# Optimization experiments

Hardware: AMD Instinct MI355X
Metric: run time of the kernel (lower is better)

Reference implementation:

```python
import jax, jax.numpy as jnp
import numpy as np

# Model dims (mamba_ssm defaults: expand=2, d_state=16, d_conv=4, dt_rank=ceil(d_model/16))
V, D_MODEL, N_LAYERS = 32000, 768, 2
D_INNER, D_STATE, D_CONV, DT_RANK = 1536, 16, 4, 48
BATCH, SEQ = 2, 2048


def setup_inputs() -> dict:
    key = jax.random.key(0)
    ks = jax.random.split(key, 10)

    def nrm(k, shape, s=0.02):
        return (jax.random.normal(k, shape) * s).astype(jnp.float32)

    x = jax.random.randint(ks[0], (BATCH, SEQ), 0, V)
    emb = nrm(ks[1], (V, D_MODEL))
    # per-layer Mamba params, stacked on leading layer axis
    W_in = nrm(ks[2], (N_LAYERS, 2 * D_INNER, D_MODEL))          # in_proj (no bias)
    conv_w = nrm(ks[3], (N_LAYERS, D_INNER, 1, D_CONV), 0.1)      # depthwise causal conv
    conv_b = jnp.zeros((N_LAYERS, D_INNER), jnp.float32)
    W_x = nrm(ks[4], (N_LAYERS, DT_RANK + 2 * D_STATE, D_INNER))  # x_proj (no bias)
    W_dt = nrm(ks[5], (N_LAYERS, D_INNER, DT_RANK), 0.05)         # dt_proj
    b_dt = jnp.full((N_LAYERS, D_INNER), -4.0, jnp.float32)       # softplus(-4) ~ small dt
    # A initialized as -exp(A_log) with A_log = log(1..d_state), per mamba_ssm
    A_log = jnp.log(jnp.broadcast_to(
        jnp.arange(1, D_STATE + 1, dtype=jnp.float32), (N_LAYERS, D_INNER, D_STATE)))
    D_skip = jnp.ones((N_LAYERS, D_INNER), jnp.float32)
    W_out = nrm(ks[6], (N_LAYERS, D_MODEL, D_INNER))              # out_proj (no bias)
    ln_g = jnp.ones((D_MODEL,), jnp.float32)
    ln_b = jnp.zeros((D_MODEL,), jnp.float32)
    head_w = nrm(ks[7], (V, D_MODEL))
    head_b = jnp.zeros((V,), jnp.float32)
    return dict(x=x, emb=emb, W_in=W_in, conv_w=conv_w, conv_b=conv_b, W_x=W_x,
                W_dt=W_dt, b_dt=b_dt, A_log=A_log, D_skip=D_skip, W_out=W_out,
                ln_g=ln_g, ln_b=ln_b, head_w=head_w, head_b=head_b)


def mamba_block(h, W_in, conv_w, conv_b, W_x, W_dt, b_dt, A_log, D_skip, W_out):
    # h: (B, L, D_MODEL)
    xz = jnp.einsum('bld,ed->ble', h, W_in)              # (B, L, 2*d_inner)
    u, z = jnp.split(xz, 2, axis=-1)
    # causal depthwise conv over time
    uc = jnp.transpose(u, (0, 2, 1))                     # (B, d_inner, L)
    uc = jax.lax.conv_general_dilated(
        uc, conv_w, window_strides=(1,), padding=[(D_CONV - 1, 0)],
        feature_group_count=D_INNER, dimension_numbers=('NCH', 'OIH', 'NCH'))
    u = jax.nn.silu(jnp.transpose(uc, (0, 2, 1)) + conv_b)
    # input-dependent dt, B, C
    x_dbl = jnp.einsum('bld,ed->ble', u, W_x)            # (B, L, dt_rank+2*d_state)
    dtl, Bm, Cm = jnp.split(x_dbl, [DT_RANK, DT_RANK + D_STATE], axis=-1)
    dt = jax.nn.softplus(jnp.einsum('blr,dr->bld', dtl, W_dt) + b_dt)  # (B, L, d_inner)
    A = -jnp.exp(A_log)                                  # (d_inner, d_state)

    def step(hst, inp):
        dt_t, u_t, B_t, C_t = inp                        # (B,d_inner),(B,d_inner),(B,d_state),(B,d_state)
        hst = jnp.exp(dt_t[..., None] * A) * hst + (dt_t * u_t)[..., None] * B_t[:, None, :]
        y_t = jnp.einsum('bds,bs->bd', hst, C_t)
        return hst, y_t

    h0 = jnp.zeros((u.shape[0], D_INNER, D_STATE), u.dtype)
    xs = (dt.transpose(1, 0, 2), u.transpose(1, 0, 2),
          Bm.transpose(1, 0, 2), Cm.transpose(1, 0, 2))
    _, ys = jax.lax.scan(step, h0, xs)                   # (L, B, d_inner)
    y = ys.transpose(1, 0, 2) + u * D_skip
    y = y * jax.nn.silu(z)
    return jnp.einsum('bli,oi->blo', y, W_out)           # back to (B, L, D_MODEL)


def reference(x, emb, W_in, conv_w, conv_b, W_x, W_dt, b_dt, A_log, D_skip,
              W_out, ln_g, ln_b, head_w, head_b):
    h = emb[x]                                           # (B, L, D_MODEL)
    for l in range(N_LAYERS):
        h = h + mamba_block(h, W_in[l], conv_w[l], conv_b[l], W_x[l], W_dt[l],
                            b_dt[l], A_log[l], D_skip[l], W_out[l])
    mu = jnp.mean(h, axis=-1, keepdims=True)
    var = jnp.mean((h - mu) ** 2, axis=-1, keepdims=True)
    hn = (h - mu) * jax.lax.rsqrt(var + 1e-5) * ln_g + ln_b
    return jnp.einsum('bld,vd->blv', hn, head_w) + head_b
```

## Files before the change

kernel.cpp:

```cpp
#include <hip/hip_runtime.h>
#include <hip/hip_bf16.h>
#include <stdint.h>

#define BL    4096
#define DM    768
#define DI    1536
#define DS    16
#define DCONV 4
#define DTR   48
#define NL    2
#define SEQL  2048
#define BATCH 2
#define VOC   32000
#define NCH   32
#define CT    64

typedef __bf16 bf16_t;
typedef __bf16 bf16x8 __attribute__((ext_vector_type(8)));
typedef __bf16 bf16x4 __attribute__((ext_vector_type(4)));
typedef float  f32x4  __attribute__((ext_vector_type(4)));

__device__ __forceinline__ float sigmoidf_(float x) { return 1.f / (1.f + __expf(-x)); }
__device__ __forceinline__ float softplus_(float x) {
  return (x > 20.f) ? x : log1pf(__expf(x));
}

__global__ __launch_bounds__(256) void k_embed(const int* __restrict__ x,
                                               const float* __restrict__ emb,
                                               float* __restrict__ h,
                                               bf16_t* __restrict__ hb) {
  int row = blockIdx.x;
  int tok = x[row];
  const float* e = emb + (size_t)tok * DM;
  float* hr = h + (size_t)row * DM;
  bf16_t* hbr = hb + (size_t)row * DM;
  for (int c = threadIdx.x; c < DM; c += 256) {
    float v = e[c];
    hr[c] = v;
    hbr[c] = (bf16_t)v;
  }
}

#define NV0 1179648L
#define NV1 589824L
#define NV2 6144000L
#define NS3 393216L
#define NS4 196608L
#define NVT (NV0 + NV1 + NV2)
#define NTOT (NVT + NS3 + NS4)

__global__ __launch_bounds__(256) void k_cvtw(const float* __restrict__ Win,
                                              const float* __restrict__ Wout,
                                              const float* __restrict__ Whead,
                                              const float* __restrict__ Wx,
                                              const float* __restrict__ Wdt,
                                              bf16_t* __restrict__ bin,
                                              bf16_t* __restrict__ bout,
                                              bf16_t* __restrict__ bhead,
                                              bf16_t* __restrict__ bx,
                                              bf16_t* __restrict__ bdt) {
  long i = (long)blockIdx.x * 256 + threadIdx.x;
  if (i >= NTOT) return;
  if (i < NVT) {
    const float* s; bf16_t* d; long j = i;
    if (i < NV0)            { s = Win;   d = bin; }
    else if (i < NV0 + NV1) { s = Wout;  d = bout;  j = i - NV0; }
    else                    { s = Whead; d = bhead; j = i - NV0 - NV1; }
    float4 v = ((const float4*)s)[j];
    bf16x4 o;
    o[0] = (bf16_t)v.x; o[1] = (bf16_t)v.y; o[2] = (bf16_t)v.z; o[3] = (bf16_t)v.w;
    ((bf16x4*)d)[j] = o;
  } else if (i < NVT + NS3) {
    long j = i - NVT;
    int l = (int)(j / (128 * 1536));
    int rr = (int)((j / 1536) % 128);
    int c = (int)(j % 1536);
    bx[j] = (bf16_t)(rr < 80 ? Wx[((long)l * 80 + rr) * 1536 + c] : 0.f);
  } else {
    long j = i - NVT - NS3;
    int l = (int)(j / (1536 * 64));
    int r = (int)((j / 64) % 1536);
    int c = (int)(j & 63);
    bdt[j] = (bf16_t)(c < DTR ? Wdt[((long)l * 1536 + r) * DTR + c] : 0.f);
  }
}

__global__ __launch_bounds__(256) void k_cvt_pad(const float* __restrict__ src,
                                                 bf16_t* __restrict__ dst,
                                                 int R, int C, int srcLd, int Cpad,
                                                 long total) {
  long i = (long)blockIdx.x * 256 + threadIdx.x;
  if (i >= total) return;
  int r = (int)(i / Cpad), c = (int)(i % Cpad);
  float v = (r < R && c < C) ? src[(size_t)r * srcLd + c] : 0.f;
  dst[i] = (bf16_t)v;
}

__global__ __launch_bounds__(256) void k_zero(float* __restrict__ p, long n4) {
  long i = (long)blockIdx.x * 256 + threadIdx.x;
  if (i < n4) ((float4*)p)[i] = (float4){0.f, 0.f, 0.f, 0.f};
}

__global__ __launch_bounds__(256) void k_conv(const float* __restrict__ xz,
                                              const float* __restrict__ cw,
                                              const float* __restrict__ cb,
                                              bf16_t* __restrict__ ucb, long total) {
  long i = (long)blockIdx.x * 256 + threadIdx.x;
  if (i >= total) return;
  int d = (int)(i % DI);
  long row = i / DI;
  int l = (int)(row % SEQL);
  const float* w = cw + (size_t)d * DCONV;
  float s = cb[d];
#pragma unroll
  for (int j = 0; j < DCONV; j++) {
    int lj = l - (DCONV - 1) + j;
    if (lj >= 0) s += xz[(row - (DCONV - 1) + j) * (2 * DI) + d] * w[j];
  }
  float v = s * sigmoidf_(s);
  ucb[i] = (bf16_t)v;
}

__global__ __launch_bounds__(256) void k_scan1(const float* __restrict__ dt,
                                               const bf16_t* __restrict__ uc,
                                               const float* __restrict__ xdbl,
                                               const float* __restrict__ A_log,
                                               float* __restrict__ cA,
                                               float* __restrict__ cB) {
  int gi = blockIdx.x * 256 + threadIdx.x;
  int s = gi & 15;
  int rest = gi >> 4;
  int d = rest % DI;
  int rest2 = rest / DI;
  int c = rest2 % NCH;
  int b = rest2 / NCH;
  float a = -__expf(A_log[d * DS + s]);
  long l0 = (long)c * CT;
  const float*  dtp = dt + ((long)b * SEQL + l0) * DI + d;
  const bf16_t* ucp = uc + ((long)b * SEQL + l0) * DI + d;
  const float*  Bp  = xdbl + ((long)b * SEQL + l0) * 80 + DTR + s;
  float S = 0.f, hh = 0.f;
#pragma unroll 4
  for (int l = 0; l < CT; l++) {
    float dtv = dtp[(long)l * DI];
    float uv  = (float)ucp[(long)l * DI];
    float Bv  = Bp[(long)l * 80];
    S += dtv;
    hh = __expf(dtv * a) * hh + (dtv * uv) * Bv;
  }
  cA[gi] = __expf(a * S);
  cB[gi] = hh;
}

__global__ __launch_bounds__(256) void k_scan2(const float* __restrict__ cA,
                                               const float* __restrict__ cB,
                                               float* __restrict__ hst) {
  int gj = blockIdx.x * 256 + threadIdx.x;
  int ds_ = gj & (DI * DS - 1);
  int b = gj / (DI * DS);
  float h = 0.f;
#pragma unroll
  for (int c = 0; c < NCH; c++) {
    long idx = ((long)(b * NCH + c) * DI * DS) + ds_;
    hst[idx] = h;
    h = cA[idx] * h + cB[idx];
  }
}

__global__ __launch_bounds__(256) void k_scan3g(const float* __restrict__ dt,
                                                const bf16_t* uc,
                                                const float* __restrict__ xdbl,
                                                const float* __restrict__ A_log,
                                                const float* __restrict__ hst,
                                                const float* __restrict__ xz,
                                                const float* __restrict__ Dsk,
                                                bf16_t* o) {
  int gi = blockIdx.x * 256 + threadIdx.x;
  int s = gi & 15;
  int rest = gi >> 4;
  int d = rest % DI;
  int rest2 = rest / DI;
  int c = rest2 % NCH;
  int b = rest2 / NCH;
  float a = -__expf(A_log[d * DS + s]);
  float dval = Dsk[d];
  long l0 = (long)c * CT;
  const float*  dtp = dt + ((long)b * SEQL + l0) * DI + d;
  const bf16_t* ucp = uc + ((long)b * SEQL + l0) * DI + d;
  const float*  Bp  = xdbl + ((long)b * SEQL + l0) * 80 + DTR + s;
  const float*  Cp  = Bp + DS;
  const float*  zp  = xz + ((long)b * SEQL + l0) * (2 * DI) + DI + d;
  bf16_t* yp = o + ((long)b * SEQL + l0) * DI + d;
  float h = hst[gi];
#pragma unroll 4
  for (int l = 0; l < CT; l++) {
    float dtv = dtp[(long)l * DI];
    float uv  = (float)ucp[(long)l * DI];
    float Bv  = Bp[(long)l * 80];
    float Cv  = Cp[(long)l * 80];
    h = __expf(dtv * a) * h + (dtv * uv) * Bv;
    float y = h * Cv;
    y += __shfl_xor(y, 1);
    y += __shfl_xor(y, 2);
    y += __shfl_xor(y, 4);
    y += __shfl_xor(y, 8);
    if (s == 0) {
      float z = zp[(long)l * 2 * DI];
      float yy = (y + uv * dval) * z * sigmoidf_(z);
      yp[(long)l * DI] = (bf16_t)yy;
    }
  }
}

__global__ __launch_bounds__(256) void k_ln(const float* __restrict__ h,
                                            const float* __restrict__ g,
                                            const float* __restrict__ bta,
                                            bf16_t* __restrict__ o) {
  __shared__ float sm[4];
  int row = blockIdx.x;
  int t = threadIdx.x;
  const float* hr = h + (long)row * DM;
  float v0 = hr[t], v1 = hr[t + 256], v2 = hr[t + 512];
  float s = v0 + v1 + v2;
#pragma unroll
  for (int off = 32; off > 0; off >>= 1) s += __shfl_down(s, off);
  if ((t & 63) == 0) sm[t >> 6] = s;
  __syncthreads();
  float mu = (sm[0] + sm[1] + sm[2] + sm[3]) * (1.f / DM);
  __syncthreads();
  float d0 = v0 - mu, d1 = v1 - mu, d2 = v2 - mu;
  float q = d0 * d0 + d1 * d1 + d2 * d2;
#pragma unroll
  for (int off = 32; off > 0; off >>= 1) q += __shfl_down(q, off);
  if ((t & 63) == 0) sm[t >> 6] = q;
  __syncthreads();
  float var = (sm[0] + sm[1] + sm[2] + sm[3]) * (1.f / DM);
  float rs = rsqrtf(var + 1e-5f);
  bf16_t* orow = o + (long)row * DM;
  orow[t]       = (bf16_t)(d0 * rs * g[t]       + bta[t]);
  orow[t + 256] = (bf16_t)(d1 * rs * g[t + 256] + bta[t + 256]);
  orow[t + 512] = (bf16_t)(d2 * rs * g[t + 512] + bta[t + 512]);
}

__device__ __forceinline__ void stage16(const bf16_t* gp, bf16_t* lp) {
  __builtin_amdgcn_global_load_lds(
      (const __attribute__((address_space(1))) uint32_t*)gp,
      (__attribute__((address_space(3))) uint32_t*)lp, 16, 0, 0);
}

template <int EPI>
__global__ __launch_bounds__(256) void k_gemm(const bf16_t* __restrict__ A,
                                              const bf16_t* __restrict__ W,
                                              float* __restrict__ C,
                                              const float* __restrict__ bias,
                                              bf16_t* __restrict__ side,
                                              int M, int N, int K, int ldc) {
  __shared__ char smem[16384];
  bf16_t* lA = (bf16_t*)smem;
  bf16_t* lB = (bf16_t*)(smem + 8192);
  const int tid = threadIdx.x;
  const int lane = tid & 63;
  const int wv = tid >> 6;
  const int wm = wv >> 1, wn = wv & 1;
  const long m0 = (long)blockIdx.y * 128;
  const long n0 = (long)blockIdx.x * 128;
  const int r0 = tid >> 2;
  const int c8 = (tid & 3) * 8;
  const int fr = lane & 15;
  const int kq = lane >> 4;

  f32x4 acc[4][4];
#pragma unroll
  for (int i = 0; i < 4; i++)
#pragma unroll
    for (int j = 0; j < 4; j++) acc[i][j] = (f32x4){0.f, 0.f, 0.f, 0.f};

  const bf16_t* Ab = A + (m0 + r0) * (long)K + c8;
  const bf16_t* Wb = W + (n0 + r0) * (long)K + c8;
  bf16_t* lAp = lA + r0 * 32 + c8;
  bf16_t* lBp = lB + r0 * 32 + c8;
  const long s64K = 64L * K;

  for (int k0 = 0; k0 < K; k0 += 32) {
    __syncthreads();
    stage16(Ab + k0, lAp);
    stage16(Ab + k0 + s64K, lAp + 64 * 32);
    stage16(Wb + k0, lBp);
    stage16(Wb + k0 + s64K, lBp + 64 * 32);
    __syncthreads();
    bf16x8 af[4], bfv[4];
#pragma unroll
    for (int f = 0; f < 4; f++)
      af[f] = *(const bf16x8*)&lA[(wm * 64 + f * 16 + fr) * 32 + kq * 8];
#pragma unroll
    for (int f = 0; f < 4; f++)
      bfv[f] = *(const bf16x8*)&lB[(wn * 64 + f * 16 + fr) * 32 + kq * 8];
#pragma unroll
    for (int fm = 0; fm < 4; fm++)
#pragma unroll
      for (int fn = 0; fn < 4; fn++)
        acc[fm][fn] = __builtin_amdgcn_mfma_f32_16x16x32_bf16(af[fm], bfv[fn],
                                                              acc[fm][fn], 0, 0, 0);
  }

  {
    float* lf = (float*)smem;
    const int q = lane >> 4;
    const int cc = lane & 15;
    const int colt = (tid & 31) * 4;
    float4 bias4 = {0.f, 0.f, 0.f, 0.f};
    if (EPI == 3) bias4 = *(const float4*)&bias[n0 + colt];
#pragma unroll
    for (int p = 0; p < 4; ++p) {
      __syncthreads();
      if (wm == (p >> 1)) {
#pragma unroll
        for (int fl = 0; fl < 2; ++fl) {
          int fm = (p & 1) * 2 + fl;
#pragma unroll
          for (int fn = 0; fn < 4; ++fn) {
            f32x4 v = acc[fm][fn];
            float* dst = &lf[(fl * 16 + q * 4) * 128 + wn * 64 + fn * 16 + cc];
#pragma unroll
            for (int r = 0; r < 4; ++r) dst[r * 128] = v[r];
          }
        }
      }
      __syncthreads();
      const long rowg0 = m0 + p * 32;
#pragma unroll
      for (int it = 0; it < 4; ++it) {
        int rl = it * 8 + (tid >> 5);
        f32x4 v = *(const f32x4*)&lf[rl * 128 + colt];
        long row = rowg0 + rl;
        long cg = n0 + colt;
        float* gp = &C[row * (long)ldc + cg];
        if (EPI == 3) {
          v[0] = softplus_(v[0] + bias4.x);
          v[1] = softplus_(v[1] + bias4.y);
          v[2] = softplus_(v[2] + bias4.z);
          v[3] = softplus_(v[3] + bias4.w);
          *(f32x4*)gp = v;
        } else {
          f32x4 c0 = *(const f32x4*)gp;
          v[0] += c0[0]; v[1] += c0[1]; v[2] += c0[2]; v[3] += c0[3];
          *(f32x4*)gp = v;
          bf16x4 s4;
          s4[0] = (bf16_t)v[0]; s4[1] = (bf16_t)v[1];
          s4[2] = (bf16_t)v[2]; s4[3] = (bf16_t)v[3];
          *(bf16x4*)&side[row * (long)ldc + cg] = s4;
        }
      }
    }
  }
}

__global__ __launch_bounds__(256) void k_gemm_sk(const bf16_t* __restrict__ A,
                                                 const bf16_t* __restrict__ W,
                                                 float* __restrict__ C,
                                                 int N, int K, int KS, int ldc) {
  __shared__ bf16_t lA[128 * 32];
  __shared__ bf16_t lB[128 * 32];
  const int tid = threadIdx.x;
  const int lane = tid & 63;
  const int wv = tid >> 6;
  const int wm = wv >> 1, wn = wv & 1;
  const long m0 = (long)blockIdx.y * 128;
  const long n0 = (long)blockIdx.x * 128;
  const int kLo = blockIdx.z * KS;
  const int r0 = tid >> 2;
  const int c8 = (tid & 3) * 8;
  const int fr = lane & 15;
  const int kq = lane >> 4;

  f32x4 acc[4][4];
#pragma unroll
  for (int i = 0; i < 4; i++)
#pragma unroll
    for (int j = 0; j < 4; j++) acc[i][j] = (f32x4){0.f, 0.f, 0.f, 0.f};

  const bf16_t* Ab = A + (m0 + r0) * (long)K + c8;
  const bf16_t* Wb = W + (n0 + r0) * (long)K + c8;
  bf16_t* lAp = lA + r0 * 32 + c8;
  bf16_t* lBp = lB + r0 * 32 + c8;
  const long s64K = 64L * K;

  for (int k0 = kLo; k0 < kLo + KS; k0 += 32) {
    __syncthreads();
    stage16(Ab + k0, lAp);
    stage16(Ab + k0 + s64K, lAp + 64 * 32);
    stage16(Wb + k0, lBp);
    stage16(Wb + k0 + s64K, lBp + 64 * 32);
    __syncthreads();
    bf16x8 af[4], bfv[4];
#pragma unroll
    for (int f = 0; f < 4; f++)
      af[f] = *(const bf16x8*)&lA[(wm * 64 + f * 16 + fr) * 32 + kq * 8];
#pragma unroll
    for (int f = 0; f < 4; f++)
      bfv[f] = *(const bf16x8*)&lB[(wn * 64 + f * 16 + fr) * 32 + kq * 8];
#pragma unroll
    for (int fm = 0; fm < 4; fm++)
#pragma unroll
      for (int fn = 0; fn < 4; fn++)
        acc[fm][fn] = __builtin_amdgcn_mfma_f32_16x16x32_bf16(af[fm], bfv[fn],
                                                              acc[fm][fn], 0, 0, 0);
  }

  const int r4 = (lane >> 4) * 4;
  const int cc = lane & 15;
#pragma unroll
  for (int fm = 0; fm < 4; fm++) {
    long rowb = m0 + wm * 64 + fm * 16 + r4;
#pragma unroll
    for (int fn = 0; fn < 4; fn++) {
      long col = n0 + wn * 64 + fn * 16 + cc;
      if (col < N) {
#pragma unroll
        for (int r = 0; r < 4; r++)
          atomicAdd(&C[(rowb + r) * (long)ldc + col], acc[fm][fn][r]);
      }
    }
  }
}


#define GLD256(ab, j, ktt, pp) do {                                             \
    int idx_ = (j) * 512 + tid;                                                 \
    int r_ = idx_ >> 3; int c16_ = idx_ & 7;                                    \
    size_t col_ = (size_t)(ktt) * 64 + (size_t)((c16_ ^ (r_ & 7)) << 3);        \
    const bf16_t* gp_ = (ab) ? (Wp + ((size_t)(n0 + r_)) * K + col_)            \
                             : (Ap + ((size_t)(m0 + r_)) * K + col_);           \
    bf16_t* lp_ = lds + ((((pp) * 2 + (ab)) * 256 + r_) * 64) + c16_ * 8;       \
    __builtin_amdgcn_global_load_lds(                                           \
        (const __attribute__((address_space(1))) uint32_t*)gp_,                 \
        (__attribute__((address_space(3))) uint32_t*)lp_, 16, 0, 0);            \
  } while (0)

#define STAGE_ALL(pp, ktt) do {                                                 \
    GLD256(0, 0, ktt, pp); GLD256(0, 2, ktt, pp);                               \
    GLD256(1, 0, ktt, pp); GLD256(1, 1, ktt, pp);                               \
    GLD256(1, 2, ktt, pp); GLD256(1, 3, ktt, pp);                               \
    GLD256(0, 1, ktt, pp); GLD256(0, 3, ktt, pp);                               \
  } while (0)

#define COMPUTE256(pp, mg, kh) do {                                             \
    const char* lb_ = (const char*)lds;                                         \
    bf16x8 af_[4], bv_[4];                                                      \
    _Pragma("unroll") for (int f = 0; f < 4; ++f) {                             \
      int row_ = wm * 128 + (mg) * 64 + f * 16 + fr;                            \
      int byte_ = (((pp) * 2 + 0) * 256 + row_) * 128 +                         \
                  (((kh) * 64 + kq * 16) ^ ((row_ & 7) << 4));                  \
      af_[f] = *(const bf16x8*)(lb_ + byte_);                                   \
    }                                                                           \
    _Pragma("unroll") for (int f = 0; f < 4; ++f) {                             \
      int row_ = wn * 64 + f * 16 + fr;                                         \
      int byte_ = (((pp) * 2 + 1) * 256 + row_) * 128 +                         \
                  (((kh) * 64 + kq * 16) ^ ((row_ & 7) << 4));                  \
      bv_[f] = *(const bf16x8*)(lb_ + byte_);                                   \
    }                                                                           \
    __builtin_amdgcn_s_setprio(1);                                              \
    _Pragma("unroll") for (int fm = 0; fm < 4; ++fm)                            \
      _Pragma("unroll") for (int fn = 0; fn < 4; ++fn)                          \
        acc[(mg) * 4 + fm][fn] = __builtin_amdgcn_mfma_f32_16x16x32_bf16(       \
            af_[fm], bv_[fn], acc[(mg) * 4 + fm][fn], 0, 0, 0);                 \
    __builtin_amdgcn_s_setprio(0);                                              \
  } while (0)

#define WAITV8()  asm volatile("s_waitcnt vmcnt(8)" ::: "memory")
#define WAITV2()  asm volatile("s_waitcnt vmcnt(2)" ::: "memory")
#define WAITV0()  asm volatile("s_waitcnt vmcnt(0)" ::: "memory")
#define BARRIER() do { __builtin_amdgcn_s_barrier();                            \
                       asm volatile("" ::: "memory"); } while (0)

template <int EPI>
__global__ __launch_bounds__(512, 2) void k_gemm256(const bf16_t* __restrict__ Ap,
                                                    const bf16_t* __restrict__ Wp,
                                                    float* __restrict__ C,
                                                    const float* __restrict__ bias,
                                                    int K, int ldc) {
  __shared__ bf16_t lds[2 * 2 * 256 * 64];
  const int tid = threadIdx.x;
  const int lane = tid & 63;
  const int wid = tid >> 6;
  const int wm = wid >> 2, wn = wid & 3;
  const int fr = lane & 15, kq = lane >> 4;

  const int cpx = gridDim.x >> 3;
  const int wg = ((int)blockIdx.x & 7) * cpx + ((int)blockIdx.x >> 3);
  const long m0 = (long)(wg & 15) * 256;
  const long n0 = (long)(wg >> 4) * 256;

  f32x4 acc[8][4];
#pragma unroll
  for (int i = 0; i < 8; i++)
#pragma unroll
    for (int j = 0; j < 4; j++) acc[i][j] = (f32x4){0.f, 0.f, 0.f, 0.f};

  STAGE_ALL(0, 0);
  WAITV2();
  BARRIER();

  const int NT = K >> 6;
  for (int kt = 0; kt < NT; ++kt) {
    const int p = kt & 1;
    const bool pre = (kt + 1 < NT);
    if (pre) STAGE_ALL(p ^ 1, kt + 1);
    COMPUTE256(p, 0, 0);
    if (pre) WAITV8(); else WAITV0();
    BARRIER();
    COMPUTE256(p, 1, 0);
    COMPUTE256(p, 0, 1);
    COMPUTE256(p, 1, 1);
    if (pre) {
      WAITV2();
      BARRIER();
    }
  }

  {
    float* lf = (float*)(void*)lds;
    const int q = lane >> 4;
    const int cc = lane & 15;
    float4 bias4 = {0.f, 0.f, 0.f, 0.f};
    if (EPI == 1) bias4 = *(const float4*)&bias[n0 + lane * 4];
#pragma unroll
    for (int p = 0; p < 4; ++p) {
      __syncthreads();
      if (wm == (p >> 1)) {
        const int mgb = (p & 1) * 4;
#pragma unroll
        for (int m4 = 0; m4 < 4; ++m4)
#pragma unroll
          for (int n = 0; n < 4; ++n) {
            f32x4 v = acc[mgb + m4][n];
            float* dst = &lf[(m4 * 16 + q * 4) * 260 + wn * 64 + n * 16 + cc];
#pragma unroll
            for (int r = 0; r < 4; ++r) dst[r * 260] = v[r];
          }
      }
      __syncthreads();
      const long rowg0 = m0 + p * 64;
#pragma unroll
      for (int it = 0; it < 8; ++it) {
        int row_loc = wid * 8 + it;
        f32x4 v = *(const f32x4*)&lf[row_loc * 260 + lane * 4];
        float* gp = &C[(rowg0 + row_loc) * (long)ldc + n0 + lane * 4];
        if (EPI == 1) {
          v[0] += bias4.x; v[1] += bias4.y; v[2] += bias4.z; v[3] += bias4.w;
          __builtin_nontemporal_store(v, (f32x4*)gp);
        } else {
          *(f32x4*)gp = v;
        }
      }
    }
  }
}

static inline int cdiv_l(long a, long b) { return (int)((a + b - 1) / b); }

extern "C" void kernel_launch(void* const* d_in, const int* in_sizes, int n_in,
                              void* d_out, int out_size, void* d_ws, size_t ws_size,
                              hipStream_t stream) {
  (void)in_sizes; (void)n_in; (void)out_size; (void)ws_size;
  const int*   x      = (const int*)  d_in[0];
  const float* emb    = (const float*)d_in[1];
  const float* W_in   = (const float*)d_in[2];
  const float* conv_w = (const float*)d_in[3];
  const float* conv_b = (const float*)d_in[4];
  const float* W_x    = (const float*)d_in[5];
  const float* W_dt   = (const float*)d_in[6];
  const float* b_dt   = (const float*)d_in[7];
  const float* A_log  = (const float*)d_in[8];
  const float* D_skip = (const float*)d_in[9];
  const float* W_out  = (const float*)d_in[10];
  const float* ln_g   = (const float*)d_in[11];
  const float* ln_b   = (const float*)d_in[12];
  const float* head_w = (const float*)d_in[13];
  const float* head_b = (const float*)d_in[14];
  float* out = (float*)d_out;

  bf16_t* abuf   = (bf16_t*)d_ws;
  bf16_t* hbf    = abuf   + (size_t)BL * DI;
  bf16_t* dtl    = hbf    + (size_t)BL * DM;
  bf16_t* wb_in  = dtl    + (size_t)BL * 64;
  bf16_t* wb_out = wb_in  + (size_t)2 * 3072 * 768;
  bf16_t* wb_hd  = wb_out + (size_t)2 * 768 * 1536;
  bf16_t* wb_x   = wb_hd  + (size_t)VOC * DM;
  bf16_t* wb_dt  = wb_x   + (size_t)2 * 128 * 1536;

  float* xz   = out;
  float* xdbl = xz   + (size_t)BL * 2 * DI;
  float* dtb  = xdbl + (size_t)BL * 80;
  float* h    = dtb  + (size_t)BL * DI;
  float* cA   = h    + (size_t)BL * DM;
  float* cB   = cA   + (size_t)BATCH * NCH * DI * DS;
  float* hst  = cB   + (size_t)BATCH * NCH * DI * DS;

  const int scan_blocks = BATCH * NCH * DI * DS / 256;
  const int st_blocks   = BATCH * DI * DS / 256;

  k_cvtw<<<cdiv_l(NTOT, 256), 256, 0, stream>>>(W_in, W_out, head_w, W_x, W_dt,
                                                wb_in, wb_out, wb_hd, wb_x, wb_dt);
  k_embed<<<BL, 256, 0, stream>>>(x, emb, h, hbf);

  for (int l = 0; l < NL; ++l) {
    k_gemm256<0><<<(BL / 256) * (2 * DI / 256), 512, 0, stream>>>(
        hbf, wb_in + (size_t)l * 3072 * 768, xz, nullptr, DM, 2 * DI);
    k_conv<<<cdiv_l((long)BL * DI, 256), 256, 0, stream>>>(
        xz, conv_w + (size_t)l * DI * DCONV, conv_b + (size_t)l * DI,
        abuf, (long)BL * DI);
    k_zero<<<cdiv_l((long)BL * 80 / 4, 256), 256, 0, stream>>>(xdbl, (long)BL * 80 / 4);
    k_gemm_sk<<<dim3(1, BL / 128, 4), 256, 0, stream>>>(
        abuf, wb_x + (size_t)l * 128 * 1536, xdbl, 80, DI, DI / 4, 80);
    k_cvt_pad<<<cdiv_l((long)BL * 64, 256), 256, 0, stream>>>(
        xdbl, dtl, BL, DTR, 80, 64, (long)BL * 64);
    k_gemm<3><<<dim3(DI / 128, BL / 128), 256, 0, stream>>>(
        dtl, wb_dt + (size_t)l * 1536 * 64, dtb, b_dt + (size_t)l * DI, nullptr,
        BL, DI, 64, DI);
    k_scan1<<<scan_blocks, 256, 0, stream>>>(dtb, abuf, xdbl,
                                             A_log + (size_t)l * DI * DS, cA, cB);
    k_scan2<<<st_blocks, 256, 0, stream>>>(cA, cB, hst);
    k_scan3g<<<scan_blocks, 256, 0, stream>>>(dtb, abuf, xdbl,
                                              A_log + (size_t)l * DI * DS, hst,
                                              xz, D_skip + (size_t)l * DI, abuf);
    k_gemm<5><<<dim3(DM / 128, BL / 128), 256, 0, stream>>>(
        abuf, wb_out + (size_t)l * 768 * 1536, h, nullptr, hbf, BL, DM, DI, DM);
  }

  k_ln<<<BL, 256, 0, stream>>>(h, ln_g, ln_b, abuf);
  k_gemm256<1><<<(BL / 256) * (VOC / 256), 512, 0, stream>>>(
      abuf, wb_hd, out, head_b, DM, VOC);
}
```

Baseline: 1.043 ms.

## Unify all GEMMs on a double-buffered swizzled 128x128 kernel

Replaces both the simple 128x128 GEMM (single-buffered, K step 32) and the 256x256 head/in_proj GEMM with one 128x128 kernel. The new kernel double-buffers 64-wide K tiles into XOR-swizzled LDS, raises MFMA issue priority and uses grouped block-to-tile mapping. This speeds up the small dt/out_proj GEMMs through prefetching and fewer barriers. It also moves the large vocab-head and in_proj GEMMs to smaller tiles, which lowers operand reuse per block but gives more blocks and higher occupancy.

```diff
diff --git a/kernel.cpp b/kernel.cpp
--- a/kernel.cpp
+++ b/kernel.cpp
@@ -248,26 +248,70 @@
       (__attribute__((address_space(3))) uint32_t*)lp, 16, 0, 0);
 }
 
+
+#define GLD128(ab, j, ktt, pp) do {                                             \
+    int idx_ = (j) * 256 + tid;                                                 \
+    int r_ = idx_ >> 3; int c16_ = idx_ & 7;                                    \
+    size_t col_ = (size_t)(ktt) * 64 + (size_t)((c16_ ^ (r_ & 7)) << 3);        \
+    const bf16_t* gp_ = (ab) ? (Wp + ((size_t)(n0 + r_)) * K + col_)            \
+                             : (Ap + ((size_t)(m0 + r_)) * K + col_);           \
+    bf16_t* lp_ = lds + ((((pp) * 2 + (ab)) * 128 + r_) * 64) + c16_ * 8;       \
+    stage16(gp_, lp_);                                                          \
+  } while (0)
+
+#define STAGE8(pp, ktt) do {                                                    \
+    GLD128(0, 0, ktt, pp); GLD128(0, 1, ktt, pp);                               \
+    GLD128(0, 2, ktt, pp); GLD128(0, 3, ktt, pp);                               \
+    GLD128(1, 0, ktt, pp); GLD128(1, 1, ktt, pp);                               \
+    GLD128(1, 2, ktt, pp); GLD128(1, 3, ktt, pp);                               \
+  } while (0)
+
+#define COMPUTE128(pp, kh) do {                                                 \
+    const char* lb_ = (const char*)lds;                                         \
+    bf16x8 af_[4], bv_[4];                                                      \
+    _Pragma("unroll") for (int f = 0; f < 4; ++f) {                             \
+      int row_ = wm * 64 + f * 16 + fr;                                         \
+      int byte_ = (((pp) * 2 + 0) * 128 + row_) * 128 +                         \
+                  (((kh) * 64 + kq * 16) ^ ((row_ & 7) << 4));                  \
+      af_[f] = *(const bf16x8*)(lb_ + byte_);                                   \
+    }                                                                           \
+    _Pragma("unroll") for (int f = 0; f < 4; ++f) {                             \
+      int row_ = wn * 64 + f * 16 + fr;                                         \
+      int byte_ = (((pp) * 2 + 1) * 128 + row_) * 128 +                         \
+                  (((kh) * 64 + kq * 16) ^ ((row_ & 7) << 4));                  \
+      bv_[f] = *(const bf16x8*)(lb_ + byte_);                                   \
+    }                                                                           \
+    __builtin_amdgcn_s_setprio(1);                                              \
+    _Pragma("unroll") for (int fm = 0; fm < 4; ++fm)                            \
+      _Pragma("unroll") for (int fn = 0; fn < 4; ++fn)                          \
+        acc[fm][fn] = __builtin_amdgcn_mfma_f32_16x16x32_bf16(                  \
+            af_[fm], bv_[fn], acc[fm][fn], 0, 0, 0);                            \
+    __builtin_amdgcn_s_setprio(0);                                              \
+  } while (0)
+
+#define WAITV8()  asm volatile("s_waitcnt vmcnt(8)" ::: "memory")
+#define WAITV0()  asm volatile("s_waitcnt vmcnt(0)" ::: "memory")
+#define BARRIER() do { __builtin_amdgcn_s_barrier();                            \
+                       asm volatile("" ::: "memory"); } while (0)
+
 template <int EPI>
-__global__ __launch_bounds__(256) void k_gemm(const bf16_t* __restrict__ A,
-                                              const bf16_t* __restrict__ W,
-                                              float* __restrict__ C,
-                                              const float* __restrict__ bias,
-                                              bf16_t* __restrict__ side,
-                                              int M, int N, int K, int ldc) {
-  __shared__ char smem[16384];
-  bf16_t* lA = (bf16_t*)smem;
-  bf16_t* lB = (bf16_t*)(smem + 8192);
+__global__ __launch_bounds__(256, 2) void k_gemm128(const bf16_t* __restrict__ Ap,
+                                                    const bf16_t* __restrict__ Wp,
+                                                    float* __restrict__ C,
+                                                    const float* __restrict__ bias,
+                                                    bf16_t* __restrict__ side,
+                                                    int K, int ldc) {
+  __shared__ bf16_t lds[2 * 2 * 128 * 64];
   const int tid = threadIdx.x;
   const int lane = tid & 63;
   const int wv = tid >> 6;
   const int wm = wv >> 1, wn = wv & 1;
-  const long m0 = (long)blockIdx.y * 128;
-  const long n0 = (long)blockIdx.x * 128;
-  const int r0 = tid >> 2;
-  const int c8 = (tid & 3) * 8;
-  const int fr = lane & 15;
-  const int kq = lane >> 4;
+  const int fr = lane & 15, kq = lane >> 4;
+
+  const int cpx = gridDim.x >> 3;
+  const int wg = ((int)blockIdx.x & 7) * cpx + ((int)blockIdx.x >> 3);
+  const long m0 = (long)(wg & 31) * 128;
+  const long n0 = (long)(wg >> 5) * 128;
 
   f32x4 acc[4][4];
 #pragma unroll
@@ -275,41 +319,26 @@
 #pragma unroll
     for (int j = 0; j < 4; j++) acc[i][j] = (f32x4){0.f, 0.f, 0.f, 0.f};
 
-  const bf16_t* Ab = A + (m0 + r0) * (long)K + c8;
-  const bf16_t* Wb = W + (n0 + r0) * (long)K + c8;
-  bf16_t* lAp = lA + r0 * 32 + c8;
-  bf16_t* lBp = lB + r0 * 32 + c8;
-  const long s64K = 64L * K;
-
-  for (int k0 = 0; k0 < K; k0 += 32) {
-    __syncthreads();
-    stage16(Ab + k0, lAp);
-    stage16(Ab + k0 + s64K, lAp + 64 * 32);
-    stage16(Wb + k0, lBp);
-    stage16(Wb + k0 + s64K, lBp + 64 * 32);
-    __syncthreads();
-    bf16x8 af[4], bfv[4];
-#pragma unroll
-    for (int f = 0; f < 4; f++)
-      af[f] = *(const bf16x8*)&lA[(wm * 64 + f * 16 + fr) * 32 + kq * 8];
-#pragma unroll
-    for (int f = 0; f < 4; f++)
-      bfv[f] = *(const bf16x8*)&lB[(wn * 64 + f * 16 + fr) * 32 + kq * 8];
-#pragma unroll
-    for (int fm = 0; fm < 4; fm++)
-#pragma unroll
-      for (int fn = 0; fn < 4; fn++)
-        acc[fm][fn] = __builtin_amdgcn_mfma_f32_16x16x32_bf16(af[fm], bfv[fn],
-                                                              acc[fm][fn], 0, 0, 0);
+  STAGE8(0, 0);
+  const int NT = K >> 6;
+  for (int kt = 0; kt < NT; ++kt) {
+    const int p = kt & 1;
+    const bool pre = (kt + 1 < NT);
+    if (pre) STAGE8(p ^ 1, kt + 1);
+    if (pre) WAITV8(); else WAITV0();
+    BARRIER();
+    COMPUTE128(p, 0);
+    COMPUTE128(p, 1);
+    BARRIER();
   }
 
   {
-    float* lf = (float*)smem;
+    float* lf = (float*)(void*)lds;
     const int q = lane >> 4;
     const int cc = lane & 15;
     const int colt = (tid & 31) * 4;
     float4 bias4 = {0.f, 0.f, 0.f, 0.f};
-    if (EPI == 3) bias4 = *(const float4*)&bias[n0 + colt];
+    if (EPI == 1 || EPI == 3) bias4 = *(const float4*)&bias[n0 + colt];
 #pragma unroll
     for (int p = 0; p < 4; ++p) {
       __syncthreads();
@@ -335,7 +364,12 @@
         long row = rowg0 + rl;
         long cg = n0 + colt;
         float* gp = &C[row * (long)ldc + cg];
-        if (EPI == 3) {
+        if (EPI == 0) {
+          *(f32x4*)gp = v;
+        } else if (EPI == 1) {
+          v[0] += bias4.x; v[1] += bias4.y; v[2] += bias4.z; v[3] += bias4.w;
+          __builtin_nontemporal_store(v, (f32x4*)gp);
+        } else if (EPI == 3) {
           v[0] = softplus_(v[0] + bias4.x);
           v[1] = softplus_(v[1] + bias4.y);
           v[2] = softplus_(v[2] + bias4.z);
@@ -419,139 +453,6 @@
 #pragma unroll
         for (int r = 0; r < 4; r++)
           atomicAdd(&C[(rowb + r) * (long)ldc + col], acc[fm][fn][r]);
-      }
-    }
-  }
-}
-
-
-#define GLD256(ab, j, ktt, pp) do {                                             \
-    int idx_ = (j) * 512 + tid;                                                 \
-    int r_ = idx_ >> 3; int c16_ = idx_ & 7;                                    \
-    size_t col_ = (size_t)(ktt) * 64 + (size_t)((c16_ ^ (r_ & 7)) << 3);        \
-    const bf16_t* gp_ = (ab) ? (Wp + ((size_t)(n0 + r_)) * K + col_)            \
-                             : (Ap + ((size_t)(m0 + r_)) * K + col_);           \
-    bf16_t* lp_ = lds + ((((pp) * 2 + (ab)) * 256 + r_) * 64) + c16_ * 8;       \
-    __builtin_amdgcn_global_load_lds(                                           \
-        (const __attribute__((address_space(1))) uint32_t*)gp_,                 \
-        (__attribute__((address_space(3))) uint32_t*)lp_, 16, 0, 0);            \
-  } while (0)
-
-#define STAGE_ALL(pp, ktt) do {                                                 \
-    GLD256(0, 0, ktt, pp); GLD256(0, 2, ktt, pp);                               \
-    GLD256(1, 0, ktt, pp); GLD256(1, 1, ktt, pp);                               \
-    GLD256(1, 2, ktt, pp); GLD256(1, 3, ktt, pp);                               \
-    GLD256(0, 1, ktt, pp); GLD256(0, 3, ktt, pp);                               \
-  } while (0)
-
-#define COMPUTE256(pp, mg, kh) do {                                             \
-    const char* lb_ = (const char*)lds;                                         \
-    bf16x8 af_[4], bv_[4];                                                      \
-    _Pragma("unroll") for (int f = 0; f < 4; ++f) {                             \
-      int row_ = wm * 128 + (mg) * 64 + f * 16 + fr;                            \
-      int byte_ = (((pp) * 2 + 0) * 256 + row_) * 128 +                         \
-                  (((kh) * 64 + kq * 16) ^ ((row_ & 7) << 4));                  \
-      af_[f] = *(const bf16x8*)(lb_ + byte_);                                   \
-    }                                                                           \
-    _Pragma("unroll") for (int f = 0; f < 4; ++f) {                             \
-      int row_ = wn * 64 + f * 16 + fr;                                         \
-      int byte_ = (((pp) * 2 + 1) * 256 + row_) * 128 +                         \
-                  (((kh) * 64 + kq * 16) ^ ((row_ & 7) << 4));                  \
-      bv_[f] = *(const bf16x8*)(lb_ + byte_);                                   \
-    }                                                                           \
-    __builtin_amdgcn_s_setprio(1);                                              \
-    _Pragma("unroll") for (int fm = 0; fm < 4; ++fm)                            \
-      _Pragma("unroll") for (int fn = 0; fn < 4; ++fn)                          \
-        acc[(mg) * 4 + fm][fn] = __builtin_amdgcn_mfma_f32_16x16x32_bf16(       \
-            af_[fm], bv_[fn], acc[(mg) * 4 + fm][fn], 0, 0, 0);                 \
-    __builtin_amdgcn_s_setprio(0);                                              \
-  } while (0)
-
-#define WAITV8()  asm volatile("s_waitcnt vmcnt(8)" ::: "memory")
-#define WAITV2()  asm volatile("s_waitcnt vmcnt(2)" ::: "memory")
-#define WAITV0()  asm volatile("s_waitcnt vmcnt(0)" ::: "memory")
-#define BARRIER() do { __builtin_amdgcn_s_barrier();                            \
-                       asm volatile("" ::: "memory"); } while (0)
-
-template <int EPI>
-__global__ __launch_bounds__(512, 2) void k_gemm256(const bf16_t* __restrict__ Ap,
-                                                    const bf16_t* __restrict__ Wp,
-                                                    float* __restrict__ C,
-                                                    const float* __restrict__ bias,
-                                                    int K, int ldc) {
-  __shared__ bf16_t lds[2 * 2 * 256 * 64];
-  const int tid = threadIdx.x;
-  const int lane = tid & 63;
-  const int wid = tid >> 6;
-  const int wm = wid >> 2, wn = wid & 3;
-  const int fr = lane & 15, kq = lane >> 4;
-
-  const int cpx = gridDim.x >> 3;
-  const int wg = ((int)blockIdx.x & 7) * cpx + ((int)blockIdx.x >> 3);
-  const long m0 = (long)(wg & 15) * 256;
-  const long n0 = (long)(wg >> 4) * 256;
-
-  f32x4 acc[8][4];
-#pragma unroll
-  for (int i = 0; i < 8; i++)
-#pragma unroll
-    for (int j = 0; j < 4; j++) acc[i][j] = (f32x4){0.f, 0.f, 0.f, 0.f};
-
-  STAGE_ALL(0, 0);
-  WAITV2();
-  BARRIER();
-
-  const int NT = K >> 6;
-  for (int kt = 0; kt < NT; ++kt) {
-    const int p = kt & 1;
-    const bool pre = (kt + 1 < NT);
-    if (pre) STAGE_ALL(p ^ 1, kt + 1);
-    COMPUTE256(p, 0, 0);
-    if (pre) WAITV8(); else WAITV0();
-    BARRIER();
-    COMPUTE256(p, 1, 0);
-    COMPUTE256(p, 0, 1);
-    COMPUTE256(p, 1, 1);
-    if (pre) {
-      WAITV2();
-      BARRIER();
-    }
-  }
-
-  {
-    float* lf = (float*)(void*)lds;
-    const int q = lane >> 4;
-    const int cc = lane & 15;
-    float4 bias4 = {0.f, 0.f, 0.f, 0.f};
-    if (EPI == 1) bias4 = *(const float4*)&bias[n0 + lane * 4];
-#pragma unroll
-    for (int p = 0; p < 4; ++p) {
-      __syncthreads();
-      if (wm == (p >> 1)) {
-        const int mgb = (p & 1) * 4;
-#pragma unroll
-        for (int m4 = 0; m4 < 4; ++m4)
-#pragma unroll
-          for (int n = 0; n < 4; ++n) {
-            f32x4 v = acc[mgb + m4][n];
-            float* dst = &lf[(m4 * 16 + q * 4) * 260 + wn * 64 + n * 16 + cc];
-#pragma unroll
-            for (int r = 0; r < 4; ++r) dst[r * 260] = v[r];
-          }
-      }
-      __syncthreads();
-      const long rowg0 = m0 + p * 64;
-#pragma unroll
-      for (int it = 0; it < 8; ++it) {
-        int row_loc = wid * 8 + it;
-        f32x4 v = *(const f32x4*)&lf[row_loc * 260 + lane * 4];
-        float* gp = &C[(rowg0 + row_loc) * (long)ldc + n0 + lane * 4];
-        if (EPI == 1) {
-          v[0] += bias4.x; v[1] += bias4.y; v[2] += bias4.z; v[3] += bias4.w;
-          __builtin_nontemporal_store(v, (f32x4*)gp);
-        } else {
-          *(f32x4*)gp = v;
-        }
       }
     }
   }
@@ -605,8 +506,8 @@
   k_embed<<<BL, 256, 0, stream>>>(x, emb, h, hbf);
 
   for (int l = 0; l < NL; ++l) {
-    k_gemm256<0><<<(BL / 256) * (2 * DI / 256), 512, 0, stream>>>(
-        hbf, wb_in + (size_t)l * 3072 * 768, xz, nullptr, DM, 2 * DI);
+    k_gemm128<0><<<(BL / 128) * (2 * DI / 128), 256, 0, stream>>>(
+        hbf, wb_in + (size_t)l * 3072 * 768, xz, nullptr, nullptr, DM, 2 * DI);
     k_conv<<<cdiv_l((long)BL * DI, 256), 256, 0, stream>>>(
         xz, conv_w + (size_t)l * DI * DCONV, conv_b + (size_t)l * DI,
         abuf, (long)BL * DI);
@@ -615,20 +516,20 @@
         abuf, wb_x + (size_t)l * 128 * 1536, xdbl, 80, DI, DI / 4, 80);
     k_cvt_pad<<<cdiv_l((long)BL * 64, 256), 256, 0, stream>>>(
         xdbl, dtl, BL, DTR, 80, 64, (long)BL * 64);
-    k_gemm<3><<<dim3(DI / 128, BL / 128), 256, 0, stream>>>(
+    k_gemm128<3><<<(BL / 128) * (DI / 128), 256, 0, stream>>>(
         dtl, wb_dt + (size_t)l * 1536 * 64, dtb, b_dt + (size_t)l * DI, nullptr,
-        BL, DI, 64, DI);
+        64, DI);
     k_scan1<<<scan_blocks, 256, 0, stream>>>(dtb, abuf, xdbl,
                                              A_log + (size_t)l * DI * DS, cA, cB);
     k_scan2<<<st_blocks, 256, 0, stream>>>(cA, cB, hst);
     k_scan3g<<<scan_blocks, 256, 0, stream>>>(dtb, abuf, xdbl,
                                               A_log + (size_t)l * DI * DS, hst,
                                               xz, D_skip + (size_t)l * DI, abuf);
-    k_gemm<5><<<dim3(DM / 128, BL / 128), 256, 0, stream>>>(
-        abuf, wb_out + (size_t)l * 768 * 1536, h, nullptr, hbf, BL, DM, DI, DM);
+    k_gemm128<5><<<(BL / 128) * (DM / 128), 256, 0, stream>>>(
+        abuf, wb_out + (size_t)l * 768 * 1536, h, nullptr, hbf, DI, DM);
   }
 
   k_ln<<<BL, 256, 0, stream>>>(h, ln_g, ln_b, abuf);
-  k_gemm256<1><<<(BL / 256) * (VOC / 256), 512, 0, stream>>>(
-      abuf, wb_hd, out, head_b, DM, VOC);
-}
+  k_gemm128<1><<<(BL / 128) * (VOC / 128), 256, 0, stream>>>(
+      abuf, wb_hd, out, head_b, nullptr, DM, VOC);
+}
```

Result: slower. 1.072 ms (+2.8%).
